# Kernel optimization log

Measured on AMD Instinct MI355X. Metric: run time of the kernel, lower is better.

The kernel has to match this reference:

```python
import jax, jax.numpy as jnp
import numpy as np

B, C_IN, T, N = 16, 64, 12, 1024
KS, C_OUT = 3, 64


def setup_inputs() -> dict:
    key = jax.random.key(0)
    k1, k2, k3 = jax.random.split(key, 3)
    x = jax.random.normal(k1, (B, C_IN, T, N), dtype=jnp.float32)
    # graph Chebyshev kernel [N, Ks*N]; scale down so matmuls stay well-conditioned
    kernel = jax.random.normal(k2, (N, KS * N), dtype=jnp.float32) / np.sqrt(N)
    # xavier-uniform theta [Ks*c_in, c_out]
    limit = np.sqrt(6.0 / (KS * C_IN + C_OUT))
    theta = jax.random.uniform(k3, (KS * C_IN, C_OUT), dtype=jnp.float32,
                               minval=-limit, maxval=limit)
    bias = jnp.zeros((C_OUT,), dtype=jnp.float32)
    return {"x": x, "kernel": kernel, "theta": theta, "bias": bias}


def reference(x, kernel, theta, bias):
    # x: [B, C, T, N]; kernel: [N, Ks*N] viewed as [N, Ks, N]; theta: [C*Ks, c_out]
    Bb, C, Tt, Nn = x.shape
    Ks = kernel.shape[1] // Nn
    Kr = kernel.reshape(Nn, Ks, Nn)            # [n, k, m]
    th = theta.reshape(C, Ks, -1)              # [c, k, o] (row index = c*Ks + k)
    # batched spectral conv over all timesteps at once (fuses the per-t loop)
    x_mul = jnp.einsum('bctn,nkm->bctkm', x, Kr)       # [B,C,T,Ks,N]
    gc = jnp.einsum('bctkm,cko->botm', x_mul, th)      # [B,c_out,T,N]
    gc = gc + bias[None, :, None, None]
    # c_in == c_out -> residual is identity
    return jax.nn.relu(gc + x)
```

## Files before the change

### kernel.cpp

```cpp
#include <hip/hip_runtime.h>

#define NB   16
#define NC   64
#define NT   12
#define NN   1024
#define NKS  3

typedef float  f32x4  __attribute__((ext_vector_type(4)));
typedef short  s16x8  __attribute__((ext_vector_type(8)));
typedef unsigned short u16x4 __attribute__((ext_vector_type(4)));
typedef unsigned short u16x8 __attribute__((ext_vector_type(8)));
typedef unsigned short ush;

__device__ __forceinline__ ush f2bf(float f) {
    union { float f; unsigned u; } v; v.f = f;
    unsigned r = v.u + 0x7FFFu + ((v.u >> 16) & 1u);
    return (ush)(r >> 16);
}
__device__ __forceinline__ float bf2f(ush h) {
    union { unsigned u; float f; } v; v.u = ((unsigned)h) << 16;
    return v.f;
}

__device__ __forceinline__ void cp16(const void* g, void* l) {
    __builtin_amdgcn_global_load_lds(
        (const __attribute__((address_space(1))) unsigned int*)g,
        (__attribute__((address_space(3))) unsigned int*)l, 16, 0, 0);
}

#define APAN_OFF 0
#define KB_OFF   25165824
#define TH_OFF   31457280

__global__ __launch_bounds__(256)
void spatio_prep(const float* __restrict__ x, const float* __restrict__ kern,
                 const float* __restrict__ theta,
                 ush* __restrict__ apan, ush* __restrict__ kb, ush* __restrict__ thbf)
{
    const int blk = blockIdx.x;
    const int tid = threadIdx.x;

    if (blk < 1536) {
        int ch   = blk * 256 + tid;
        int p    = ch & 3;
        int j    = (ch >> 2) % 192;
        int rest = (ch >> 2) / 192;
        int nb   = rest & 31, mt = rest >> 5;
        int d    = p ^ (j & 3);
        int k    = j >> 6, mm = j & 63;
        int col  = (k << 10) + (mt << 6) + mm;
        u16x8 w;
#pragma unroll
        for (int i = 0; i < 8; ++i) {
            int n = nb * 32 + d * 8 + i;
            w[i] = f2bf(kern[(size_t)n * (NKS * NN) + col]);
        }
        ((u16x8*)kb)[ch] = w;
    } else if (blk < 1584) {
        int id = (blk - 1536) * 256 + tid;
        if (id < 12288) {
            int row = id >> 6, o = id & 63;
            int c = row / 3, k = row - 3 * c;
            thbf[o * 192 + k * 64 + c] = f2bf(theta[id]);
        }
    } else {
        int id   = (blk - 1584) * 256 + tid;
        int slot = id & 511;
        int g2nb = id >> 9;
        int nb   = g2nb & 31, g2 = g2nb >> 5;
        int row  = slot >> 2, p = slot & 3;
        int d    = p ^ (row & 3);
        int bl   = row >> 6, c = row & 63;
        int bt   = 2 * g2 + bl;
        int b    = bt / NT, t = bt - NT * b;
        const float* src = x + ((size_t)((b * NC + c) * NT + t)) * NN + nb * 32 + d * 8;
        float4 a0 = ((const float4*)src)[0];
        float4 a1 = ((const float4*)src)[1];
        u16x8 w;
        w[0] = f2bf(a0.x); w[1] = f2bf(a0.y); w[2] = f2bf(a0.z); w[3] = f2bf(a0.w);
        w[4] = f2bf(a1.x); w[5] = f2bf(a1.y); w[6] = f2bf(a1.z); w[7] = f2bf(a1.w);
        ((u16x8*)apan)[id] = w;
    }
}

__global__ __launch_bounds__(256, 2)
void spatio_main(const ush* __restrict__ apan, const ush* __restrict__ kb,
                 const ush* __restrict__ thbf, const float* __restrict__ bias,
                 float* __restrict__ out)
{
    __shared__ __attribute__((aligned(128))) char smem[57344];
    ush (*xm)[200] = (ush (*)[200])smem;
    ush (*stL)[32] = (ush (*)[32])(smem + 40960);
    ush (*stH)[32] = (ush (*)[32])(smem + 49152);

    const int tid  = threadIdx.x;
    const int g2   = blockIdx.x;
    const int mt   = blockIdx.y;
    const int m_base = mt * 64;
    const int lane = tid & 63;
    const int wid  = tid >> 6;
    const int wr   = wid & 1;
    const int wn   = wid >> 1;
    const int quad = lane >> 4;
    const int l16  = lane & 15;
    const int pofs = (quad ^ (l16 & 3)) * 8;

    const char* apan_c = (const char*)apan + ((size_t)g2 << 18);
    const char* kb_c   = (const char*)kb + ((size_t)mt * 32 * 768 * 16);

    f32x4 acc[4][6];
#pragma unroll
    for (int i = 0; i < 4; ++i)
#pragma unroll
        for (int j = 0; j < 6; ++j) acc[i][j] = (f32x4){0.f, 0.f, 0.f, 0.f};

#pragma unroll
    for (int i = 0; i < 2; ++i)
        cp16(apan_c + (i * 256 + tid) * 16, smem + (i * 256 + tid) * 16);
#pragma unroll
    for (int i = 0; i < 3; ++i)
        cp16(kb_c + (i * 256 + tid) * 16, smem + 8192 + (i * 256 + tid) * 16);

    for (int it = 0; it < 32; ++it) {
        const int p = it & 1;
        char* buf = smem + p * 20480;
        __syncthreads();
        if (it < 31) {
            const char* asrc = apan_c + ((size_t)(it + 1) << 13);
            const char* bsrc = kb_c + (size_t)(it + 1) * 12288;
            char* nbuf = smem + (p ^ 1) * 20480;
#pragma unroll
            for (int i = 0; i < 2; ++i)
                cp16(asrc + (i * 256 + tid) * 16, nbuf + (i * 256 + tid) * 16);
#pragma unroll
            for (int i = 0; i < 3; ++i)
                cp16(bsrc + (i * 256 + tid) * 16, nbuf + 8192 + (i * 256 + tid) * 16);
        }
        if ((it >> 1) == mt) {
            const char* asrc = apan_c + ((size_t)it << 13);
            char* sb = smem + 40960 + (it & 1) * 8192;
#pragma unroll
            for (int i = 0; i < 2; ++i) {
                int m = i * 256 + tid;
                int slot = (m & ~3) + ((m & 3) ^ ((m >> 2) & 3));
                cp16(asrc + slot * 16, sb + m * 16);
            }
        }

        ush (*As)[32] = (ush (*)[32])buf;
        ush (*Bs)[32] = (ush (*)[32])(buf + 8192);
        s16x8 af[4], bf[6];
#pragma unroll
        for (int rb = 0; rb < 4; ++rb)
            af[rb] = *(const s16x8*)&As[64 * wr + 16 * rb + l16][pofs];
#pragma unroll
        for (int jb = 0; jb < 6; ++jb)
            bf[jb] = *(const s16x8*)&Bs[96 * wn + 16 * jb + l16][pofs];
#pragma unroll
        for (int rb = 0; rb < 4; ++rb)
#pragma unroll
            for (int jb = 0; jb < 6; ++jb)
                acc[rb][jb] = __builtin_amdgcn_mfma_f32_16x16x32_bf16(af[rb], bf[jb], acc[rb][jb], 0, 0, 0);
    }

    float bo[4];
#pragma unroll
    for (int r = 0; r < 4; ++r) bo[r] = bias[16 * wid + 4 * quad + r];

    for (int pass = 0; pass < 2; ++pass) {
        __syncthreads();
        if (wr == pass) {
#pragma unroll
            for (int rb = 0; rb < 4; ++rb)
#pragma unroll
                for (int jb = 0; jb < 6; ++jb) {
                    int J  = 96 * wn + 16 * jb + l16;
                    int kk = J >> 6, mm = J & 63;
                    int ck0 = kk * 64 + 16 * rb + 4 * quad;
                    u16x4 w;
                    w.x = f2bf(acc[rb][jb].x); w.y = f2bf(acc[rb][jb].y);
                    w.z = f2bf(acc[rb][jb].z); w.w = f2bf(acc[rb][jb].w);
                    *(u16x4*)&xm[mm][ck0] = w;
                }
        }
        __syncthreads();

        f32x4 acc2[4];
#pragma unroll
        for (int jb = 0; jb < 4; ++jb) acc2[jb] = (f32x4){0.f, 0.f, 0.f, 0.f};
#pragma unroll
        for (int ks = 0; ks < 6; ++ks) {
            s16x8 a2 = *(const s16x8*)(thbf + (size_t)(16 * wid + l16) * 192 + ks * 32 + quad * 8);
#pragma unroll
            for (int jb = 0; jb < 4; ++jb) {
                s16x8 b2 = *(const s16x8*)&xm[16 * jb + l16][ks * 32 + quad * 8];
                acc2[jb] = __builtin_amdgcn_mfma_f32_16x16x32_bf16(a2, b2, acc2[jb], 0, 0, 0);
            }
        }

        const int bt = 2 * g2 + pass;
        const int b2i = bt / NT, t2 = bt - NT * b2i;
#pragma unroll
        for (int jb = 0; jb < 4; ++jb) {
            int mm = 16 * jb + l16;
#pragma unroll
            for (int r = 0; r < 4; ++r) {
                int o = 16 * wid + 4 * quad + r;
                int row = pass * 64 + o;
                ush rv = (jb < 2) ? stL[row][mm] : stH[row][mm - 32];
                size_t idx = (((size_t)(b2i * NC + o) * NT + t2) * NN) + m_base + mm;
                float v = acc2[jb][r] + bo[r] + bf2f(rv);
                out[idx] = fmaxf(v, 0.f);
            }
        }
    }
}

extern "C" void kernel_launch(void* const* d_in, const int* in_sizes, int n_in,
                              void* d_out, int out_size, void* d_ws, size_t ws_size,
                              hipStream_t stream) {
    const float* x     = (const float*)d_in[0];
    const float* kern  = (const float*)d_in[1];
    const float* theta = (const float*)d_in[2];
    const float* bias  = (const float*)d_in[3];
    float* out = (float*)d_out;
    (void)in_sizes; (void)n_in; (void)out_size; (void)ws_size;

    ush* apan = (ush*)((char*)d_ws + APAN_OFF);
    ush* kbp  = (ush*)((char*)d_ws + KB_OFF);
    ush* thbf = (ush*)((char*)d_ws + TH_OFF);

    hipLaunchKernelGGL(spatio_prep, dim3(7728), dim3(256), 0, stream,
                       x, kern, theta, apan, kbp, thbf);
    hipLaunchKernelGGL(spatio_main, dim3(96, 16), dim3(256), 0, stream,
                       apan, kbp, thbf, bias, out);
}
```

Measured before the change: 185.1 us.

## Enlarge GEMM tile to 256x192 with K=64 stages and XCD-aware block remap

Restructures the main kernel to use 512-thread workgroups covering four (b,t) slices per block, with K-steps of 64 and a wider 8-way XOR swizzle in the prepacked layouts. Global-to-LDS loads are double-buffered with explicit vmcnt waits and raw barriers, MFMA issue is wrapped in raised priority, and blocks are remapped so neighbouring tiles land on the same XCD. The residual is now read from the fp32 input instead of a bf16 copy staged in LDS, which gives up the staging path in exchange for an extra global read. The intent is to halve the number of k-iterations and barriers per block and improve operand reuse, at the cost of using one block per CU and more LDS.

```diff
diff --git a/kernel.cpp b/kernel.cpp
--- a/kernel.cpp
+++ b/kernel.cpp
@@ -16,10 +16,6 @@
     union { float f; unsigned u; } v; v.f = f;
     unsigned r = v.u + 0x7FFFu + ((v.u >> 16) & 1u);
     return (ush)(r >> 16);
-}
-__device__ __forceinline__ float bf2f(ush h) {
-    union { unsigned u; float f; } v; v.u = ((unsigned)h) << 16;
-    return v.f;
 }
 
 __device__ __forceinline__ void cp16(const void* g, void* l) {
@@ -42,38 +38,37 @@
 
     if (blk < 1536) {
         int ch   = blk * 256 + tid;
-        int p    = ch & 3;
-        int j    = (ch >> 2) % 192;
-        int rest = (ch >> 2) / 192;
-        int nb   = rest & 31, mt = rest >> 5;
-        int d    = p ^ (j & 3);
+        int rest = ch / 1536;
+        int c    = ch - rest * 1536;
+        int kt   = rest & 15, mtp = rest >> 4;
+        int j    = c >> 3, pp = c & 7;
+        int d    = pp ^ (j & 7);
         int k    = j >> 6, mm = j & 63;
-        int col  = (k << 10) + (mt << 6) + mm;
+        int col  = (k << 10) + (mtp << 6) + mm;
+        int n0   = (kt << 6) + (d << 3);
         u16x8 w;
 #pragma unroll
-        for (int i = 0; i < 8; ++i) {
-            int n = nb * 32 + d * 8 + i;
-            w[i] = f2bf(kern[(size_t)n * (NKS * NN) + col]);
-        }
+        for (int i = 0; i < 8; ++i)
+            w[i] = f2bf(kern[(size_t)(n0 + i) * (NKS * NN) + col]);
         ((u16x8*)kb)[ch] = w;
     } else if (blk < 1584) {
         int id = (blk - 1536) * 256 + tid;
         if (id < 12288) {
             int row = id >> 6, o = id & 63;
-            int c = row / 3, k = row - 3 * c;
-            thbf[o * 192 + k * 64 + c] = f2bf(theta[id]);
+            int cc = row / 3, k = row - 3 * cc;
+            thbf[o * 192 + k * 64 + cc] = f2bf(theta[id]);
         }
     } else {
-        int id   = (blk - 1584) * 256 + tid;
-        int slot = id & 511;
-        int g2nb = id >> 9;
-        int nb   = g2nb & 31, g2 = g2nb >> 5;
-        int row  = slot >> 2, p = slot & 3;
-        int d    = p ^ (row & 3);
-        int bl   = row >> 6, c = row & 63;
-        int bt   = 2 * g2 + bl;
-        int b    = bt / NT, t = bt - NT * b;
-        const float* src = x + ((size_t)((b * NC + c) * NT + t)) * NN + nb * 32 + d * 8;
+        int id  = (blk - 1584) * 256 + tid;
+        int c   = id & 2047;
+        int kt  = (id >> 11) & 15;
+        int g4  = id >> 15;
+        int row = c >> 3, pp = c & 7;
+        int d   = pp ^ (row & 7);
+        int bl  = row >> 6, cc = row & 63;
+        int bt  = g4 * 4 + bl;
+        int b   = bt / NT, t = bt - NT * b;
+        const float* src = x + ((size_t)((b * NC + cc) * NT + t)) * NN + (kt << 6) + (d << 3);
         float4 a0 = ((const float4*)src)[0];
         float4 a1 = ((const float4*)src)[1];
         u16x8 w;
@@ -83,30 +78,28 @@
     }
 }
 
-__global__ __launch_bounds__(256, 2)
+__global__ __launch_bounds__(512, 1)
 void spatio_main(const ush* __restrict__ apan, const ush* __restrict__ kb,
                  const ush* __restrict__ thbf, const float* __restrict__ bias,
-                 float* __restrict__ out)
+                 const float* __restrict__ x, float* __restrict__ out)
 {
-    __shared__ __attribute__((aligned(128))) char smem[57344];
-    ush (*xm)[200] = (ush (*)[200])smem;
-    ush (*stL)[32] = (ush (*)[32])(smem + 40960);
-    ush (*stH)[32] = (ush (*)[32])(smem + 49152);
+    __shared__ __attribute__((aligned(128))) char smem[114688];
 
     const int tid  = threadIdx.x;
-    const int g2   = blockIdx.x;
-    const int mt   = blockIdx.y;
-    const int m_base = mt * 64;
+    const int bid  = blockIdx.x;
+    const int wg   = (bid & 7) * 96 + (bid >> 3);
+    const int g4   = wg >> 4;
+    const int mt   = wg & 15;
     const int lane = tid & 63;
     const int wid  = tid >> 6;
-    const int wr   = wid & 1;
-    const int wn   = wid >> 1;
+    const int wr   = wid >> 1;
+    const int wn   = wid & 1;
     const int quad = lane >> 4;
     const int l16  = lane & 15;
-    const int pofs = (quad ^ (l16 & 3)) * 8;
-
-    const char* apan_c = (const char*)apan + ((size_t)g2 << 18);
-    const char* kb_c   = (const char*)kb + ((size_t)mt * 32 * 768 * 16);
+    const int swz  = l16 & 7;
+
+    const char* abase = (const char*)apan + ((size_t)g4 << 19);
+    const char* bbase = (const char*)kb   + ((size_t)mt * 393216);
 
     f32x4 acc[4][6];
 #pragma unroll
@@ -114,106 +107,131 @@
 #pragma unroll
         for (int j = 0; j < 6; ++j) acc[i][j] = (f32x4){0.f, 0.f, 0.f, 0.f};
 
-#pragma unroll
-    for (int i = 0; i < 2; ++i)
-        cp16(apan_c + (i * 256 + tid) * 16, smem + (i * 256 + tid) * 16);
-#pragma unroll
-    for (int i = 0; i < 3; ++i)
-        cp16(kb_c + (i * 256 + tid) * 16, smem + 8192 + (i * 256 + tid) * 16);
-
-    for (int it = 0; it < 32; ++it) {
-        const int p = it & 1;
-        char* buf = smem + p * 20480;
-        __syncthreads();
-        if (it < 31) {
-            const char* asrc = apan_c + ((size_t)(it + 1) << 13);
-            const char* bsrc = kb_c + (size_t)(it + 1) * 12288;
-            char* nbuf = smem + (p ^ 1) * 20480;
-#pragma unroll
-            for (int i = 0; i < 2; ++i)
-                cp16(asrc + (i * 256 + tid) * 16, nbuf + (i * 256 + tid) * 16);
-#pragma unroll
-            for (int i = 0; i < 3; ++i)
-                cp16(bsrc + (i * 256 + tid) * 16, nbuf + 8192 + (i * 256 + tid) * 16);
-        }
-        if ((it >> 1) == mt) {
-            const char* asrc = apan_c + ((size_t)it << 13);
-            char* sb = smem + 40960 + (it & 1) * 8192;
-#pragma unroll
-            for (int i = 0; i < 2; ++i) {
-                int m = i * 256 + tid;
-                int slot = (m & ~3) + ((m & 3) ^ ((m >> 2) & 3));
-                cp16(asrc + slot * 16, sb + m * 16);
+#define STAGE(tt, pp) do {                                                  \
+        const char* as_ = abase + ((size_t)(tt) << 15);                     \
+        const char* bs_ = bbase + (size_t)(tt) * 24576;                     \
+        char* la_ = smem + (pp) * 57344;                                    \
+        char* lb_ = la_ + 32768;                                            \
+        _Pragma("unroll")                                                   \
+        for (int i_ = 0; i_ < 4; ++i_)                                      \
+            cp16(as_ + (i_ * 512 + tid) * 16, la_ + (i_ * 512 + tid) * 16); \
+        _Pragma("unroll")                                                   \
+        for (int i_ = 0; i_ < 3; ++i_)                                      \
+            cp16(bs_ + (i_ * 512 + tid) * 16, lb_ + (i_ * 512 + tid) * 16); \
+    } while (0)
+
+    STAGE(0, 0);
+    STAGE(1, 1);
+    asm volatile("s_waitcnt vmcnt(7)" ::: "memory");
+    __builtin_amdgcn_s_barrier();
+    asm volatile("" ::: "memory");
+
+#pragma unroll 2
+    for (int t = 0; t < 16; ++t) {
+        const int p = t & 1;
+        const ush (*As)[64] = (const ush (*)[64])(smem + p * 57344);
+        const ush (*Bs)[64] = (const ush (*)[64])(smem + p * 57344 + 32768);
+        s16x8 af[4];
+#pragma unroll
+        for (int kk = 0; kk < 2; ++kk)
+#pragma unroll
+            for (int g = 0; g < 2; ++g) {
+                if (g == 0) {
+#pragma unroll
+                    for (int rb = 0; rb < 4; ++rb)
+                        af[rb] = *(const s16x8*)&As[64 * wr + 16 * rb + l16]
+                                                  [((kk * 4 + quad) ^ swz) << 3];
+                }
+                s16x8 bf[3];
+#pragma unroll
+                for (int jj = 0; jj < 3; ++jj)
+                    bf[jj] = *(const s16x8*)&Bs[96 * wn + 48 * g + 16 * jj + l16]
+                                               [((kk * 4 + quad) ^ swz) << 3];
+                __builtin_amdgcn_s_setprio(1);
+#pragma unroll
+                for (int rb = 0; rb < 4; ++rb)
+#pragma unroll
+                    for (int jj = 0; jj < 3; ++jj)
+                        acc[rb][3 * g + jj] = __builtin_amdgcn_mfma_f32_16x16x32_bf16(
+                            af[rb], bf[jj], acc[rb][3 * g + jj], 0, 0, 0);
+                __builtin_amdgcn_s_setprio(0);
+                if (!(kk == 1 && g == 1)) {
+                    asm volatile("" ::: "memory");
+                    __builtin_amdgcn_s_barrier();
+                    asm volatile("" ::: "memory");
+                }
             }
-        }
-
-        ush (*As)[32] = (ush (*)[32])buf;
-        ush (*Bs)[32] = (ush (*)[32])(buf + 8192);
-        s16x8 af[4], bf[6];
-#pragma unroll
-        for (int rb = 0; rb < 4; ++rb)
-            af[rb] = *(const s16x8*)&As[64 * wr + 16 * rb + l16][pofs];
-#pragma unroll
-        for (int jb = 0; jb < 6; ++jb)
-            bf[jb] = *(const s16x8*)&Bs[96 * wn + 16 * jb + l16][pofs];
-#pragma unroll
-        for (int rb = 0; rb < 4; ++rb)
-#pragma unroll
-            for (int jb = 0; jb < 6; ++jb)
-                acc[rb][jb] = __builtin_amdgcn_mfma_f32_16x16x32_bf16(af[rb], bf[jb], acc[rb][jb], 0, 0, 0);
-    }
-
-    float bo[4];
-#pragma unroll
-    for (int r = 0; r < 4; ++r) bo[r] = bias[16 * wid + 4 * quad + r];
-
-    for (int pass = 0; pass < 2; ++pass) {
-        __syncthreads();
-        if (wr == pass) {
-#pragma unroll
-            for (int rb = 0; rb < 4; ++rb)
-#pragma unroll
-                for (int jb = 0; jb < 6; ++jb) {
-                    int J  = 96 * wn + 16 * jb + l16;
-                    int kk = J >> 6, mm = J & 63;
-                    int ck0 = kk * 64 + 16 * rb + 4 * quad;
-                    u16x4 w;
-                    w.x = f2bf(acc[rb][jb].x); w.y = f2bf(acc[rb][jb].y);
-                    w.z = f2bf(acc[rb][jb].z); w.w = f2bf(acc[rb][jb].w);
-                    *(u16x4*)&xm[mm][ck0] = w;
-                }
-        }
-        __syncthreads();
-
-        f32x4 acc2[4];
-#pragma unroll
-        for (int jb = 0; jb < 4; ++jb) acc2[jb] = (f32x4){0.f, 0.f, 0.f, 0.f};
-#pragma unroll
-        for (int ks = 0; ks < 6; ++ks) {
-            s16x8 a2 = *(const s16x8*)(thbf + (size_t)(16 * wid + l16) * 192 + ks * 32 + quad * 8);
-#pragma unroll
-            for (int jb = 0; jb < 4; ++jb) {
-                s16x8 b2 = *(const s16x8*)&xm[16 * jb + l16][ks * 32 + quad * 8];
-                acc2[jb] = __builtin_amdgcn_mfma_f32_16x16x32_bf16(a2, b2, acc2[jb], 0, 0, 0);
-            }
-        }
-
-        const int bt = 2 * g2 + pass;
-        const int b2i = bt / NT, t2 = bt - NT * b2i;
-#pragma unroll
-        for (int jb = 0; jb < 4; ++jb) {
-            int mm = 16 * jb + l16;
+        asm volatile("s_waitcnt lgkmcnt(0)" ::: "memory");
+        __builtin_amdgcn_s_barrier();
+        asm volatile("" ::: "memory");
+        if (t < 14) {
+            STAGE(t + 2, p);
+            asm volatile("s_waitcnt vmcnt(7)" ::: "memory");
+            __builtin_amdgcn_s_barrier();
+            asm volatile("" ::: "memory");
+        } else if (t == 14) {
+            asm volatile("s_waitcnt vmcnt(0)" ::: "memory");
+            __builtin_amdgcn_s_barrier();
+            asm volatile("" ::: "memory");
+        }
+    }
+#undef STAGE
+
+    ush (*xm)[64][200] = (ush (*)[64][200])smem;
+#pragma unroll
+    for (int rb = 0; rb < 4; ++rb)
+#pragma unroll
+        for (int jb = 0; jb < 6; ++jb) {
+            int J   = 96 * wn + 16 * jb + l16;
+            int kk2 = J >> 6, mm = J & 63;
+            int ck0 = (kk2 << 6) + 16 * rb + (quad << 2);
+            u16x4 w;
+            w.x = f2bf(acc[rb][jb].x); w.y = f2bf(acc[rb][jb].y);
+            w.z = f2bf(acc[rb][jb].z); w.w = f2bf(acc[rb][jb].w);
+            *(u16x4*)&xm[wr][mm][ck0] = w;
+        }
+    __syncthreads();
+
+    const int bt2 = wid & 3, hh = wid >> 2;
+    f32x4 acc2[4][2];
+#pragma unroll
+    for (int i = 0; i < 4; ++i) {
+        acc2[i][0] = (f32x4){0.f, 0.f, 0.f, 0.f};
+        acc2[i][1] = (f32x4){0.f, 0.f, 0.f, 0.f};
+    }
+#pragma unroll
+    for (int ks = 0; ks < 6; ++ks) {
+        s16x8 b2[2];
+#pragma unroll
+        for (int jm = 0; jm < 2; ++jm)
+            b2[jm] = *(const s16x8*)&xm[bt2][(hh << 5) + (jm << 4) + l16]
+                                            [(ks << 5) + (quad << 3)];
+#pragma unroll
+        for (int of = 0; of < 4; ++of) {
+            s16x8 a2 = *(const s16x8*)(thbf + (size_t)((of << 4) + l16) * 192
+                                            + (ks << 5) + (quad << 3));
+#pragma unroll
+            for (int jm = 0; jm < 2; ++jm)
+                acc2[of][jm] = __builtin_amdgcn_mfma_f32_16x16x32_bf16(
+                    a2, b2[jm], acc2[of][jm], 0, 0, 0);
+        }
+    }
+
+    const int bt = (g4 << 2) + bt2;
+    const int b  = bt / NT, tt = bt - NT * b;
+#pragma unroll
+    for (int of = 0; of < 4; ++of)
+#pragma unroll
+        for (int jm = 0; jm < 2; ++jm) {
+            int mm = (hh << 5) + (jm << 4) + l16;
 #pragma unroll
             for (int r = 0; r < 4; ++r) {
-                int o = 16 * wid + 4 * quad + r;
-                int row = pass * 64 + o;
-                ush rv = (jb < 2) ? stL[row][mm] : stH[row][mm - 32];
-                size_t idx = (((size_t)(b2i * NC + o) * NT + t2) * NN) + m_base + mm;
-                float v = acc2[jb][r] + bo[r] + bf2f(rv);
+                int o = (of << 4) + (quad << 2) + r;
+                size_t idx = ((size_t)((b * NC + o) * NT + tt)) * NN + (mt << 6) + mm;
+                float v = acc2[of][jm][r] + bias[o] + x[idx];
                 out[idx] = fmaxf(v, 0.f);
             }
         }
-    }
 }
 
 extern "C" void kernel_launch(void* const* d_in, const int* in_sizes, int n_in,
@@ -232,6 +250,6 @@
 
     hipLaunchKernelGGL(spatio_prep, dim3(7728), dim3(256), 0, stream,
                        x, kern, theta, apan, kbp, thbf);
-    hipLaunchKernelGGL(spatio_main, dim3(96, 16), dim3(256), 0, stream,
-                       apan, kbp, thbf, bias, out);
-}
+    hipLaunchKernelGGL(spatio_main, dim3(768), dim3(512), 0, stream,
+                       apan, kbp, thbf, bias, x, out);
+}
```

Result: slower. 206.0 us (+11.3%).
